# Kernel tuning notes

Measured on AMD Instinct MI355X. Metric: run time of the kernel, lower is better.

Reference implementation:

```python
import jax, jax.numpy as jnp
import numpy as np

N_QUBITS = 20
N_BLOCKS = 3
C64 = jnp.complex64


def _u3(theta, phi, lam):
    # U3(theta, phi, lam) = [[cos(t/2), -e^{i lam} sin(t/2)],
    #                        [e^{i phi} sin(t/2), e^{i(phi+lam)} cos(t/2)]]
    ct = jnp.cos(theta / 2).astype(C64)
    st = jnp.sin(theta / 2).astype(C64)
    el = jnp.exp(1j * lam.astype(C64))
    ep = jnp.exp(1j * phi.astype(C64))
    return jnp.stack([jnp.stack([ct, -el * st]),
                      jnp.stack([ep * st, ep * el * ct])])


def _cu3(theta, phi, lam):
    # controlled-U3: identity on control=|0>, U3 on control=|1>
    u = _u3(theta, phi, lam)
    m = jnp.zeros((4, 4), C64)
    m = m.at[:2, :2].set(jnp.eye(2, dtype=C64))
    m = m.at[2:, 2:].set(u)
    return m


def _apply1(psi, m, q):
    # psi: (2,)*N_QUBITS complex state tensor; apply 2x2 gate on qubit q
    psi = jnp.moveaxis(psi, q, 0).reshape(2, -1)
    psi = m @ psi
    return jnp.moveaxis(psi.reshape((2,) * N_QUBITS), 0, q)


def _apply2(psi, m4, c, t):
    # apply 4x4 gate on (control c, target t)
    psi = jnp.moveaxis(psi, (c, t), (0, 1)).reshape(4, -1)
    psi = m4 @ psi
    return jnp.moveaxis(psi.reshape((2,) * N_QUBITS), (0, 1), (c, t))


def _forward(u3_params, cu3_params):
    psi = jnp.zeros((2,) * N_QUBITS, C64).at[(0,) * N_QUBITS].set(1.0)
    for k in range(N_BLOCKS):
        for q in range(N_QUBITS):
            psi = _apply1(psi, _u3(*u3_params[k, q]), q)
        for q in range(N_QUBITS):  # circular CU3 ring: (q, (q+1) % n)
            psi = _apply2(psi, _cu3(*cu3_params[k, q]), q, (q + 1) % N_QUBITS)
    probs = (jnp.abs(psi) ** 2).reshape(2 ** N_QUBITS, 1)
    easy_scale_coeff = 2.0 ** (N_QUBITS - 1)
    gamma, beta, alpha = 0.1, 0.8, 0.3
    x = (beta * jnp.tanh(gamma * easy_scale_coeff * probs)) ** alpha
    return x - jnp.mean(x)


def setup_inputs() -> dict:
    key = jax.random.key(0)
    k1, k2 = jax.random.split(key)
    u3_params = jax.random.normal(k1, (N_BLOCKS, N_QUBITS, 3), dtype=jnp.float32)
    cu3_params = jax.random.normal(k2, (N_BLOCKS, N_QUBITS, 3), dtype=jnp.float32)
    return {"u3_params": u3_params, "cu3_params": cu3_params}


def reference(u3_params, cu3_params):
    return _forward(u3_params, cu3_params)
```

## Files before the change

kernel.cpp:

```cpp
#include <hip/hip_runtime.h>
#include <cstdint>
#include <cstddef>


#define NB 512
#define NT 512
#define SW(i) ((i) ^ (((i) >> 3) & 1u))

__device__ __forceinline__ float2 cmadd2(float2 m0, float2 a0, float2 m1, float2 a1) {
  float2 r;
  r.x = m0.x * a0.x - m0.y * a0.y + m1.x * a1.x - m1.y * a1.y;
  r.y = m0.x * a0.y + m0.y * a0.x + m1.x * a1.y + m1.y * a1.x;
  return r;
}
__device__ __forceinline__ float2 cmul(float2 a, float2 b) {
  return make_float2(a.x * b.x - a.y * b.y, a.x * b.y + a.y * b.x);
}
__device__ __forceinline__ float2 cadd(float2 a, float2 b) {
  return make_float2(a.x + b.x, a.y + b.y);
}

__device__ __forceinline__ void applyU3b0(float2* v, const float2* m) {
  float2 m00 = m[0], m01 = m[1], m10 = m[2], m11 = m[3];
  float2 a0 = v[0], a1 = v[1];
  v[0] = cmadd2(m00, a0, m01, a1); v[1] = cmadd2(m10, a0, m11, a1);
  a0 = v[2]; a1 = v[3];
  v[2] = cmadd2(m00, a0, m01, a1); v[3] = cmadd2(m10, a0, m11, a1);
}
__device__ __forceinline__ void applyF(float2* v, const float2* W0, const float2* W1) {
  float2 a0 = v[0], a1 = v[2];
  v[0] = cmadd2(W0[0], a0, W0[1], a1); v[2] = cmadd2(W0[2], a0, W0[3], a1);
  a0 = v[1]; a1 = v[3];
  v[1] = cmadd2(W1[0], a0, W1[1], a1); v[3] = cmadd2(W1[2], a0, W1[3], a1);
}
__device__ __forceinline__ void applyC(float2* v, const float2* u) {
  float2 a0 = v[1], a1 = v[3];
  v[1] = cmadd2(u[0], a0, u[1], a1); v[3] = cmadd2(u[2], a0, u[3], a1);
}

__device__ __forceinline__ float xval(float2 a) {
  float p = a.x * a.x + a.y * a.y;
  return powf(0.8f * tanhf(52428.8f * p), 0.3f);
}

__device__ __forceinline__ void mat_from(const float* s, float2* m) {
  float st, ct, sl, cl, sp, cp, spl, cpl;
  sincosf(0.5f * s[0], &st, &ct);
  sincosf(s[2], &sl, &cl);
  sincosf(s[1], &sp, &cp);
  sincosf(s[1] + s[2], &spl, &cpl);
  m[0] = make_float2(ct, 0.f);
  m[1] = make_float2(-cl * st, -sl * st);
  m[2] = make_float2(cp * st, sp * st);
  m[3] = make_float2(cpl * ct, spl * ct);
}

template <int TYPE, int INIT, int FINAL>
__global__ __launch_bounds__(NT, 4) void pass_k(const float* __restrict__ u3p,
                                                const float* __restrict__ cu3p, int k,
                                                const float2* __restrict__ in,
                                                float2* __restrict__ outPsi,
                                                float* __restrict__ accum,
                                                float* __restrict__ out) {
  __shared__ float4 A4[1024], B4[1024];
  __shared__ float2 M[168];
  __shared__ float red[8];
  unsigned t = threadIdx.x, b = blockIdx.x;

  float2 v[4];
  if (INIT) {
    v[0] = v[1] = v[2] = v[3] = make_float2(0.f, 0.f);
    if (b == 0 && t == 0) { v[0] = make_float2(1.f, 0.f); *accum = 0.f; }
  } else {
    const float4* in4 = (const float4*)in + ((size_t)b << 10) + 2u * t;
    float4 f0 = in4[0], f1 = in4[1];
    v[0] = make_float2(f0.x, f0.y); v[1] = make_float2(f0.z, f0.w);
    v[2] = make_float2(f1.x, f1.y); v[3] = make_float2(f1.z, f1.w);
  }

  float2* MU = M;
  float2* MC = M + 80;
  if (t < 20) {
    mat_from(u3p + (k * 20 + t) * 3, MU + 4 * t);
  } else if (t >= 64 && t < 84) {
    unsigned c = t - 64;
    float2 u[4];
    mat_from(cu3p + (k * 20 + c) * 3, u);
    if (c == 19) {
      MC[76] = u[0]; MC[77] = u[1]; MC[78] = u[2]; MC[79] = u[3];
    } else {
      float2 ut[4];
      mat_from(u3p + (k * 20 + c + 1) * 3, ut);
      MC[4 * c + 0] = cadd(cmul(u[0], ut[0]), cmul(u[1], ut[2]));
      MC[4 * c + 1] = cadd(cmul(u[0], ut[1]), cmul(u[1], ut[3]));
      MC[4 * c + 2] = cadd(cmul(u[2], ut[0]), cmul(u[3], ut[2]));
      MC[4 * c + 3] = cadd(cmul(u[2], ut[1]), cmul(u[3], ut[3]));
    }
  }
  __syncthreads();

#pragma unroll
  for (int p = 0; p < 10; ++p) {
    if (TYPE == 0) {
      if (p == 0) applyU3b0(v, MU);
      applyF(v, MU + 4 * (p + 1), MC + 4 * p);
    } else {
      if (p < 9) applyF(v, MU + 4 * (11 + p), MC + 4 * (10 + p));
      else       applyC(v, MC + 4 * 19);
    }
    if (p < 9) {
      float4* buf = (p & 1) ? B4 : A4;
      buf[SW(t)]        = make_float4(v[0].x, v[0].y, v[2].x, v[2].y);
      buf[SW(t + 512u)] = make_float4(v[1].x, v[1].y, v[3].x, v[3].y);
      __syncthreads();
      float4 fa = buf[SW(2u * t)], fb = buf[SW(2u * t + 1u)];
      v[0] = make_float2(fa.x, fa.y); v[1] = make_float2(fa.z, fa.w);
      v[2] = make_float2(fb.x, fb.y); v[3] = make_float2(fb.z, fb.w);
    }
  }

  if (!FINAL) {
    float4* o4 = (float4*)outPsi;
    unsigned base = b + ((t & 1u) << 9) + ((t >> 1) << 10);
    o4[base]              = make_float4(v[0].x, v[0].y, v[2].x, v[2].y);
    o4[base + (1u << 18)] = make_float4(v[1].x, v[1].y, v[3].x, v[3].y);
  } else {
    float xv0 = xval(v[0]), xv1 = xval(v[1]), xv2 = xval(v[2]), xv3 = xval(v[3]);
    float s = xv0 + xv1 + xv2 + xv3;
    float2* o2 = (float2*)out;
    unsigned rt = __brev(t) >> 23, rb = __brev(b) >> 23;
    unsigned base = rt + (rb << 9);
    o2[base] = make_float2(xv0, xv1);
    o2[base + (1u << 18)] = make_float2(xv2, xv3);
#pragma unroll
    for (int o = 32; o > 0; o >>= 1) s += __shfl_down(s, o);
    if ((t & 63u) == 0) red[t >> 6] = s;
    __syncthreads();
    if (t == 0) {
      float tot = 0.f;
#pragma unroll
      for (int i = 0; i < 8; i++) tot += red[i];
      atomicAdd(accum, tot);
    }
  }
}

__global__ void fin_k(float* __restrict__ out, const float* __restrict__ accum) {
  unsigned i = blockIdx.x * blockDim.x + threadIdx.x;
  float mean = *accum * (1.f / 1048576.f);
  float4* o4 = (float4*)out;
  float4 x = o4[i];
  x.x -= mean; x.y -= mean; x.z -= mean; x.w -= mean;
  o4[i] = x;
}

extern "C" void kernel_launch(void* const* d_in, const int* in_sizes, int n_in,
                              void* d_out, int out_size, void* d_ws, size_t ws_size,
                              hipStream_t stream) {
  const float* u3p = (const float*)d_in[0];
  const float* cu3p = (const float*)d_in[1];
  float* out = (float*)d_out;

  char* ws = (char*)d_ws;
  float2* psiA = (float2*)ws;
  float2* psiB = (float2*)(ws + (size_t)8 * 1024 * 1024);
  float* accum = (float*)(ws + (size_t)16 * 1024 * 1024);

  pass_k<0, 1, 0><<<NB, NT, 0, stream>>>(u3p, cu3p, 0, nullptr, psiB, accum, out);
  pass_k<1, 0, 0><<<NB, NT, 0, stream>>>(u3p, cu3p, 0, psiB, psiA, accum, out);
  pass_k<0, 0, 0><<<NB, NT, 0, stream>>>(u3p, cu3p, 1, psiA, psiB, accum, out);
  pass_k<1, 0, 0><<<NB, NT, 0, stream>>>(u3p, cu3p, 1, psiB, psiA, accum, out);
  pass_k<0, 0, 0><<<NB, NT, 0, stream>>>(u3p, cu3p, 2, psiA, psiB, accum, out);
  pass_k<1, 0, 1><<<NB, NT, 0, stream>>>(u3p, cu3p, 2, psiB, nullptr, accum, out);
  fin_k<<<1024, 256, 0, stream>>>(out, accum);
}
```

Baseline: 135.4 us.

## Fuse first two passes by exploiting sparse initial state per block

Replaces the first two full-state passes of block 0 with one kernel. Because the initial state is |0...0>, after the first pass only the low 10-qubit subspace is non-zero, so each block recomputes that 1024-element subspace locally and then seeds its own slice for the second pass. This removes one 8 MB write and read of the state vector and one kernel launch, at the cost of every block redundantly doing the first-pass gate work.

```diff
diff --git a/kernel.cpp b/kernel.cpp
--- a/kernel.cpp
+++ b/kernel.cpp
@@ -55,31 +55,8 @@
   m[3] = make_float2(cpl * ct, spl * ct);
 }
 
-template <int TYPE, int INIT, int FINAL>
-__global__ __launch_bounds__(NT, 4) void pass_k(const float* __restrict__ u3p,
-                                                const float* __restrict__ cu3p, int k,
-                                                const float2* __restrict__ in,
-                                                float2* __restrict__ outPsi,
-                                                float* __restrict__ accum,
-                                                float* __restrict__ out) {
-  __shared__ float4 A4[1024], B4[1024];
-  __shared__ float2 M[168];
-  __shared__ float red[8];
-  unsigned t = threadIdx.x, b = blockIdx.x;
-
-  float2 v[4];
-  if (INIT) {
-    v[0] = v[1] = v[2] = v[3] = make_float2(0.f, 0.f);
-    if (b == 0 && t == 0) { v[0] = make_float2(1.f, 0.f); *accum = 0.f; }
-  } else {
-    const float4* in4 = (const float4*)in + ((size_t)b << 10) + 2u * t;
-    float4 f0 = in4[0], f1 = in4[1];
-    v[0] = make_float2(f0.x, f0.y); v[1] = make_float2(f0.z, f0.w);
-    v[2] = make_float2(f1.x, f1.y); v[3] = make_float2(f1.z, f1.w);
-  }
-
-  float2* MU = M;
-  float2* MC = M + 80;
+__device__ __forceinline__ void load_mats(const float* u3p, const float* cu3p,
+                                          int k, unsigned t, float2* MU, float2* MC) {
   if (t < 20) {
     mat_from(u3p + (k * 20 + t) * 3, MU + 4 * t);
   } else if (t >= 64 && t < 84) {
@@ -97,6 +74,30 @@
       MC[4 * c + 3] = cadd(cmul(u[2], ut[1]), cmul(u[3], ut[3]));
     }
   }
+}
+
+template <int TYPE, int FINAL>
+__global__ __launch_bounds__(NT, 4) void pass_k(const float* __restrict__ u3p,
+                                                const float* __restrict__ cu3p, int k,
+                                                const float2* __restrict__ in,
+                                                float2* __restrict__ outPsi,
+                                                float* __restrict__ accum,
+                                                float* __restrict__ out) {
+  __shared__ float4 A4[1024], B4[1024];
+  __shared__ float2 M[168];
+  __shared__ float red[8];
+  unsigned t = threadIdx.x, b = blockIdx.x;
+
+  float2 v[4];
+  {
+    const float4* in4 = (const float4*)in + ((size_t)b << 10) + 2u * t;
+    float4 f0 = in4[0], f1 = in4[1];
+    v[0] = make_float2(f0.x, f0.y); v[1] = make_float2(f0.z, f0.w);
+    v[2] = make_float2(f1.x, f1.y); v[3] = make_float2(f1.z, f1.w);
+  }
+  float2* MU = M;
+  float2* MC = M + 80;
+  load_mats(u3p, cu3p, k, t, MU, MC);
   __syncthreads();
 
 #pragma unroll
@@ -145,6 +146,73 @@
   }
 }
 
+__global__ __launch_bounds__(NT, 4) void init2_k(const float* __restrict__ u3p,
+                                                 const float* __restrict__ cu3p,
+                                                 float2* __restrict__ outPsi,
+                                                 float* __restrict__ accum) {
+  __shared__ float4 A4[1024], B4[1024];
+  __shared__ float2 M[168];
+  unsigned t = threadIdx.x, b = blockIdx.x;
+
+  float2 v[4];
+  v[0] = v[1] = v[2] = v[3] = make_float2(0.f, 0.f);
+  if (t == 0) v[0] = make_float2(1.f, 0.f);
+  if (b == 0 && t == 0) *accum = 0.f;
+
+  float2* MU = M;
+  float2* MC = M + 80;
+  load_mats(u3p, cu3p, 0, t, MU, MC);
+  __syncthreads();
+
+#pragma unroll
+  for (int p = 0; p < 10; ++p) {
+    if (p == 0) applyU3b0(v, MU);
+    applyF(v, MU + 4 * (p + 1), MC + 4 * p);
+    if (p < 9) {
+      float4* buf = (p & 1) ? B4 : A4;
+      buf[SW(t)]        = make_float4(v[0].x, v[0].y, v[2].x, v[2].y);
+      buf[SW(t + 512u)] = make_float4(v[1].x, v[1].y, v[3].x, v[3].y);
+      __syncthreads();
+      float4 fa = buf[SW(2u * t)], fb = buf[SW(2u * t + 1u)];
+      v[0] = make_float2(fa.x, fa.y); v[1] = make_float2(fa.z, fa.w);
+      v[2] = make_float2(fb.x, fb.y); v[3] = make_float2(fb.z, fb.w);
+    }
+  }
+  float2* lds1 = (float2*)B4;
+  lds1[t]         = v[0];
+  lds1[t + 512u]  = v[1];
+  lds1[t + 1024u] = v[2];
+  lds1[t + 1536u] = v[3];
+  __syncthreads();
+
+  v[0] = v[1] = v[2] = v[3] = make_float2(0.f, 0.f);
+  if ((t & 255u) == 0) {
+    unsigned idx = (t >> 8) + (b << 1);
+    v[0] = lds1[idx];
+    v[1] = lds1[idx + 1024u];
+  }
+
+#pragma unroll
+  for (int p = 0; p < 10; ++p) {
+    if (p < 9) applyF(v, MU + 4 * (11 + p), MC + 4 * (10 + p));
+    else       applyC(v, MC + 4 * 19);
+    if (p < 9) {
+      float4* buf = (p & 1) ? B4 : A4;
+      buf[SW(t)]        = make_float4(v[0].x, v[0].y, v[2].x, v[2].y);
+      buf[SW(t + 512u)] = make_float4(v[1].x, v[1].y, v[3].x, v[3].y);
+      __syncthreads();
+      float4 fa = buf[SW(2u * t)], fb = buf[SW(2u * t + 1u)];
+      v[0] = make_float2(fa.x, fa.y); v[1] = make_float2(fa.z, fa.w);
+      v[2] = make_float2(fb.x, fb.y); v[3] = make_float2(fb.z, fb.w);
+    }
+  }
+
+  float4* o4 = (float4*)outPsi;
+  unsigned base = b + ((t & 1u) << 9) + ((t >> 1) << 10);
+  o4[base]              = make_float4(v[0].x, v[0].y, v[2].x, v[2].y);
+  o4[base + (1u << 18)] = make_float4(v[1].x, v[1].y, v[3].x, v[3].y);
+}
+
 __global__ void fin_k(float* __restrict__ out, const float* __restrict__ accum) {
   unsigned i = blockIdx.x * blockDim.x + threadIdx.x;
   float mean = *accum * (1.f / 1048576.f);
@@ -166,11 +234,10 @@
   float2* psiB = (float2*)(ws + (size_t)8 * 1024 * 1024);
   float* accum = (float*)(ws + (size_t)16 * 1024 * 1024);
 
-  pass_k<0, 1, 0><<<NB, NT, 0, stream>>>(u3p, cu3p, 0, nullptr, psiB, accum, out);
-  pass_k<1, 0, 0><<<NB, NT, 0, stream>>>(u3p, cu3p, 0, psiB, psiA, accum, out);
-  pass_k<0, 0, 0><<<NB, NT, 0, stream>>>(u3p, cu3p, 1, psiA, psiB, accum, out);
-  pass_k<1, 0, 0><<<NB, NT, 0, stream>>>(u3p, cu3p, 1, psiB, psiA, accum, out);
-  pass_k<0, 0, 0><<<NB, NT, 0, stream>>>(u3p, cu3p, 2, psiA, psiB, accum, out);
-  pass_k<1, 0, 1><<<NB, NT, 0, stream>>>(u3p, cu3p, 2, psiB, nullptr, accum, out);
+  init2_k<<<NB, NT, 0, stream>>>(u3p, cu3p, psiA, accum);
+  pass_k<0, 0><<<NB, NT, 0, stream>>>(u3p, cu3p, 1, psiA, psiB, accum, out);
+  pass_k<1, 0><<<NB, NT, 0, stream>>>(u3p, cu3p, 1, psiB, psiA, accum, out);
+  pass_k<0, 0><<<NB, NT, 0, stream>>>(u3p, cu3p, 2, psiA, psiB, accum, out);
+  pass_k<1, 1><<<NB, NT, 0, stream>>>(u3p, cu3p, 2, psiB, nullptr, accum, out);
   fin_k<<<1024, 256, 0, stream>>>(out, accum);
 }
```

Result: faster. 127.5 us (-5.8%).
